# Optimization experiments

Hardware: AMD Instinct MI355X
Metric: run time of the kernel (lower is better)

## Reference

```python
import jax, jax.numpy as jnp
import numpy as np

EPS = 1e-5  # torch BatchNorm2d default eps


def _conv1x1(x, W, b):
    # x: [B,C,H,W], W: [O,C], b: [O]
    return jnp.einsum('bchw,oc->bohw', x, W) + b[None, :, None, None]


def _bn_eval(y, gamma, beta, mean, var):
    inv = gamma / jnp.sqrt(var + EPS)
    return y * inv[None, :, None, None] + (beta - mean * inv)[None, :, None, None]


def setup_inputs() -> dict:
    key = jax.random.key(0)
    ks = jax.random.split(key, 12)
    B, C, H, W = 4, 256, 64, 64
    mid = C // 4  # k = 4
    sc_in = (2.0 / C) ** 0.5   # kaiming_normal fan_in = C for 1x1 conv
    sc_mid = (2.0 / mid) ** 0.5
    x = jax.random.normal(ks[0], (B, C, H, W), jnp.float32)
    Wf = jax.random.normal(ks[1], (mid, C), jnp.float32) * sc_in
    bf = jnp.zeros((mid,), jnp.float32)
    gamma_f = jnp.ones((mid,), jnp.float32)
    beta_f = jnp.zeros((mid,), jnp.float32)
    mean_f = jax.random.normal(ks[2], (mid,), jnp.float32) * 0.1
    var_f = jax.random.uniform(ks[3], (mid,), jnp.float32, 0.5, 1.5)
    Wg = jax.random.normal(ks[4], (mid, C), jnp.float32) * sc_in
    bg = jnp.zeros((mid,), jnp.float32)
    gamma_g = jnp.ones((mid,), jnp.float32)
    beta_g = jnp.zeros((mid,), jnp.float32)
    mean_g = jax.random.normal(ks[5], (mid,), jnp.float32) * 0.1
    var_g = jax.random.uniform(ks[6], (mid,), jnp.float32, 0.5, 1.5)
    Wh = jax.random.normal(ks[7], (mid, C), jnp.float32) * sc_in
    bh = jnp.zeros((mid,), jnp.float32)
    # v conv is constant-initialized to 0 in the original; use small random
    # weights so the attention branch contributes to the output under test.
    Wv = jax.random.normal(ks[8], (C, mid), jnp.float32) * sc_mid * 0.1
    bv = jnp.zeros((C,), jnp.float32)
    v0 = jax.random.normal(ks[9], (B, H * W, 1), jnp.float32)  # power-iter init
    return dict(x=x, Wf=Wf, bf=bf, gamma_f=gamma_f, beta_f=beta_f, mean_f=mean_f,
                var_f=var_f, Wg=Wg, bg=bg, gamma_g=gamma_g, beta_g=beta_g,
                mean_g=mean_g, var_g=var_g, Wh=Wh, bh=bh, Wv=Wv, bv=bv, v0=v0)


def reference(x, Wf, bf, gamma_f, beta_f, mean_f, var_f,
              Wg, bg, gamma_g, beta_g, mean_g, var_g,
              Wh, bh, Wv, bv, v0):
    B, C, H, W = x.shape
    mid = Wf.shape[0]
    HW = H * W
    f_x = jax.nn.relu(_bn_eval(_conv1x1(x, Wf, bf), gamma_f, beta_f, mean_f, var_f)).reshape(B, mid, HW)
    g_x = jax.nn.relu(_bn_eval(_conv1x1(x, Wg, bg), gamma_g, beta_g, mean_g, var_g)).reshape(B, mid, HW)
    h_x = _conv1x1(x, Wh, bh).reshape(B, mid, HW)
    # dense non-local correlation: [B, HW, HW]
    z = jnp.einsum('bcn,bcm->bnm', f_x, g_x)
    # power iteration (Ip=1) for spectral-norm estimate
    v = jnp.einsum('bnm,bmk->bnk', z, v0)          # [B,HW,1]
    v = v / jnp.linalg.norm(v[:, :, 0], axis=1)[:, None, None]
    s = jnp.einsum('bn,bnm,bm->b', v[:, :, 0], z, v[:, :, 0])[:, None, None]
    attn = z / s
    z2 = jnp.einsum('bnm,bcm->bcn', attn, h_x).reshape(B, mid, H, W)
    return _conv1x1(z2, Wv, bv) + x
```

## Files before the change

### kernel.cpp

```cpp
#include <hip/hip_runtime.h>

#define NB   4
#define CIN  256
#define MID  64
#define HW   4096

typedef __attribute__((ext_vector_type(8))) short bfrag8;
typedef __attribute__((ext_vector_type(4))) float facc4;

constexpr size_t OFF_FGHT  = 0;
constexpr size_t OFF_FHI   = 8388608;
constexpr size_t OFF_FLO   = 10485760;
constexpr size_t OFF_WHI   = 12582912;
constexpr size_t OFF_WLO   = 12681216;
constexpr size_t OFF_BEFF  = 12779520;
constexpr size_t OFF_W2HI  = 12780544;
constexpr size_t OFF_W2LO  = 12911616;
constexpr size_t OFF_MPART = 13042688;
constexpr size_t OFF_T     = 17236992;
constexpr size_t OFF_FGVU  = 17238016;
constexpr size_t OFF_NSQ   = 17240064;

__device__ __forceinline__ unsigned short f2bf(float f) {
    union { float f; unsigned u; } v; v.f = f;
    unsigned r = v.u + 0x7FFF + ((v.u >> 16) & 1);
    return (unsigned short)(r >> 16);
}
__device__ __forceinline__ float bf2f(unsigned short h) {
    union { unsigned u; float f; } v; v.u = ((unsigned)h) << 16;
    return v.f;
}
__device__ __forceinline__ void split_bf(float v, unsigned short& hi, unsigned short& lo) {
    hi = f2bf(v);
    lo = f2bf(v - bf2f(hi));
}

__global__ void k_weff(const float* __restrict__ Wf, const float* __restrict__ bf,
                       const float* __restrict__ gf, const float* __restrict__ btf,
                       const float* __restrict__ mf, const float* __restrict__ vf,
                       const float* __restrict__ Wg, const float* __restrict__ bg,
                       const float* __restrict__ gg, const float* __restrict__ btg,
                       const float* __restrict__ mg, const float* __restrict__ vg,
                       const float* __restrict__ Wh, const float* __restrict__ bh,
                       unsigned short* __restrict__ whi, unsigned short* __restrict__ wlo,
                       float* __restrict__ beff) {
    const int o = blockIdx.x;
    const int c = threadIdx.x;
    float w, sh;
    if (o < 64) {
        float inv = gf[o] * rsqrtf(vf[o] + 1e-5f);
        w  = Wf[o * CIN + c] * inv;
        sh = bf[o] * inv + btf[o] - mf[o] * inv;
    } else if (o < 128) {
        int oo = o - 64;
        float inv = gg[oo] * rsqrtf(vg[oo] + 1e-5f);
        w  = Wg[oo * CIN + c] * inv;
        sh = bg[oo] * inv + btg[oo] - mg[oo] * inv;
    } else {
        int oo = o - 128;
        w  = Wh[oo * CIN + c];
        sh = bh[oo];
    }
    unsigned short hi, lo; split_bf(w, hi, lo);
    whi[o * CIN + c] = hi;
    wlo[o * CIN + c] = lo;
    if (c == 0) beff[o] = sh;
}

__launch_bounds__(512)
__global__ void k_fgh2(const float* __restrict__ x,
                       const unsigned short* __restrict__ whi_g,
                       const unsigned short* __restrict__ wlo_g,
                       const float* __restrict__ beff,
                       const float* __restrict__ v0,
                       float* __restrict__ fghT,
                       unsigned short* __restrict__ fhi,
                       unsigned short* __restrict__ flo,
                       float* __restrict__ tvec,
                       float* __restrict__ mpart) {
    __shared__ unsigned short xh[64][72], xl[64][72];
    __shared__ char wbuf[2 * 192 * 72 * 2];
    unsigned short (*wh)[72] = (unsigned short(*)[72])wbuf;
    unsigned short (*wl)[72] = (unsigned short(*)[72])(wbuf + 192 * 72 * 2);

    const int nb = blockIdx.x, b = blockIdx.y;
    const int n0 = nb * 64;
    const int tid = threadIdx.x, l = tid & 63, w = tid >> 6;
    const int wo = w >> 1, wn = w & 1;
    const int lr = l & 15, lk = l >> 4;
    facc4 acc[2][3];
    #pragma unroll
    for (int i = 0; i < 2; ++i)
        #pragma unroll
        for (int j = 0; j < 3; ++j) acc[i][j] = (facc4){0.f, 0.f, 0.f, 0.f};

    const int cr = tid >> 4, nq = tid & 15;

    for (int kc = 0; kc < 4; ++kc) {
        const int c0 = kc * 64;
        {
            const float* xr = x + ((size_t)(b * CIN + c0 + cr * 2)) * HW + n0 + nq * 4;
            float4 va = *(const float4*)xr;
            float4 vb = *(const float4*)(xr + HW);
            #pragma unroll
            for (int i = 0; i < 4; ++i) {
                float fa = (&va.x)[i], fb = (&vb.x)[i];
                unsigned short ha, la, hb, lb;
                split_bf(fa, ha, la);
                split_bf(fb, hb, lb);
                const int n = nq * 4 + i;
                *(unsigned int*)&xh[n][cr * 2] = (unsigned int)ha | ((unsigned int)hb << 16);
                *(unsigned int*)&xl[n][cr * 2] = (unsigned int)la | ((unsigned int)lb << 16);
            }
        }
        {
            #pragma unroll
            for (int k = 0; k < 3; ++k) {
                const int id = tid + k * 512;
                const int orow = id >> 3, cs = id & 7;
                *(bfrag8*)&wh[orow][cs * 8] = *(const bfrag8*)(whi_g + orow * CIN + c0 + cs * 8);
                *(bfrag8*)&wl[orow][cs * 8] = *(const bfrag8*)(wlo_g + orow * CIN + c0 + cs * 8);
            }
        }
        __syncthreads();
        #pragma unroll
        for (int ks = 0; ks < 2; ++ks) {
            bfrag8 ah[2], al[2];
            #pragma unroll
            for (int s = 0; s < 2; ++s) {
                ah[s] = *(const bfrag8*)&xh[wn * 32 + s * 16 + lr][ks * 32 + lk * 8];
                al[s] = *(const bfrag8*)&xl[wn * 32 + s * 16 + lr][ks * 32 + lk * 8];
            }
            #pragma unroll
            for (int so = 0; so < 3; ++so) {
                bfrag8 bh = *(const bfrag8*)&wh[wo * 48 + so * 16 + lr][ks * 32 + lk * 8];
                bfrag8 bl = *(const bfrag8*)&wl[wo * 48 + so * 16 + lr][ks * 32 + lk * 8];
                #pragma unroll
                for (int sn = 0; sn < 2; ++sn) {
                    acc[sn][so] = __builtin_amdgcn_mfma_f32_16x16x32_bf16(ah[sn], bh, acc[sn][so], 0, 0, 0);
                    acc[sn][so] = __builtin_amdgcn_mfma_f32_16x16x32_bf16(ah[sn], bl, acc[sn][so], 0, 0, 0);
                    acc[sn][so] = __builtin_amdgcn_mfma_f32_16x16x32_bf16(al[sn], bh, acc[sn][so], 0, 0, 0);
                }
            }
        }
        __syncthreads();
    }

    float (*mls)[136]  = (float(*)[136])wbuf;
    float (*tred)[64]  = (float(*)[64])(wbuf + 36864);
    float* v0ls        = (float*)xh;

    #pragma unroll
    for (int so = 0; so < 3; ++so) {
        const int o = wo * 48 + so * 16 + lr;
        const float bias = beff[o];
        const bool rl = (o < 128);
        #pragma unroll
        for (int sn = 0; sn < 2; ++sn)
            #pragma unroll
            for (int r = 0; r < 4; ++r) {
                const int nn = wn * 32 + sn * 16 + lk * 4 + r;
                const int n = n0 + nn;
                float v = acc[sn][so][r] + bias;
                if (rl) v = fmaxf(v, 0.0f);
                if (o < 128) fghT[((size_t)(b * HW) + n) * 128 + o] = v;
                if (o < 64) {
                    unsigned short hi, lo; split_bf(v, hi, lo);
                    fhi[((size_t)(b * HW) + n) * MID + o] = hi;
                    flo[((size_t)(b * HW) + n) * MID + o] = lo;
                }
                if (o >= 64) mls[nn][o - 64] = v;
            }
    }
    if (tid < 64) v0ls[tid] = v0[(size_t)b * HW + n0 + tid];
    __syncthreads();

    {
        const int c = tid & 63, ng = tid >> 6;
        float tp = 0.f;
        #pragma unroll
        for (int i = 0; i < 8; ++i) {
            const int nn = ng * 8 + i;
            tp = fmaf(mls[nn][c], v0ls[nn], tp);
        }
        tred[ng][c] = tp;
    }
    {
        const int tcp = tid >> 4, tc = tid & 15;
        const int cp = tcp * 2, cc = tc * 4;
        float macc[2][4];
        #pragma unroll
        for (int i = 0; i < 2; ++i)
            #pragma unroll
            for (int j = 0; j < 4; ++j) macc[i][j] = 0.f;
        for (int nn = 0; nn < 64; ++nn) {
            const float g0 = mls[nn][cp], g1 = mls[nn][cp + 1];
            const float h0 = mls[nn][64 + cc + 0], h1 = mls[nn][64 + cc + 1];
            const float h2 = mls[nn][64 + cc + 2], h3 = mls[nn][64 + cc + 3];
            macc[0][0] = fmaf(g0, h0, macc[0][0]); macc[0][1] = fmaf(g0, h1, macc[0][1]);
            macc[0][2] = fmaf(g0, h2, macc[0][2]); macc[0][3] = fmaf(g0, h3, macc[0][3]);
            macc[1][0] = fmaf(g1, h0, macc[1][0]); macc[1][1] = fmaf(g1, h1, macc[1][1]);
            macc[1][2] = fmaf(g1, h2, macc[1][2]); macc[1][3] = fmaf(g1, h3, macc[1][3]);
        }
        const size_t mpb = ((size_t)(b * 64 + nb) * 64) * 64;
        *(float4*)&mpart[mpb + (size_t)(cp + 0) * 64 + cc] =
            make_float4(macc[0][0], macc[0][1], macc[0][2], macc[0][3]);
        *(float4*)&mpart[mpb + (size_t)(cp + 1) * 64 + cc] =
            make_float4(macc[1][0], macc[1][1], macc[1][2], macc[1][3]);
    }
    __syncthreads();
    if (tid < 64) {
        float s = 0.f;
        #pragma unroll
        for (int g = 0; g < 8; ++g) s += tred[g][tid];
        atomicAdd(&tvec[b * MID + tid], s);
    }
}

__launch_bounds__(256)
__global__ void k_vfg(const float* __restrict__ fghT, const float* __restrict__ t,
                      float* __restrict__ fgvu, float* __restrict__ nsq) {
    __shared__ float ts[64];
    __shared__ float vuls[256];
    __shared__ float red2[8][128];
    __shared__ float rs[4];
    const int b = blockIdx.y, n0 = blockIdx.x * 256;
    const int tid = threadIdx.x;
    if (tid < 64) ts[tid] = t[b * MID + tid];
    __syncthreads();
    const int nl = tid >> 2, q = tid & 3;
    float mynsq = 0.f;
    for (int ps = 0; ps < 4; ++ps) {
        const int n = n0 + ps * 64 + nl;
        const float* p = fghT + ((size_t)(b * HW) + n) * 128 + q * 16;
        float a = 0.f;
        #pragma unroll
        for (int u = 0; u < 4; ++u) {
            float4 fv = *(const float4*)(p + u * 4);
            a = fmaf(fv.x, ts[q * 16 + u * 4 + 0], a);
            a = fmaf(fv.y, ts[q * 16 + u * 4 + 1], a);
            a = fmaf(fv.z, ts[q * 16 + u * 4 + 2], a);
            a = fmaf(fv.w, ts[q * 16 + u * 4 + 3], a);
        }
        a += __shfl_xor(a, 1);
        a += __shfl_xor(a, 2);
        if (q == 0) { vuls[ps * 64 + nl] = a; mynsq += a * a; }
    }
    {
        float s = mynsq;
        #pragma unroll
        for (int off = 32; off > 0; off >>= 1) s += __shfl_down(s, off);
        if ((tid & 63) == 0) rs[tid >> 6] = s;
        __syncthreads();
        if (tid == 0) atomicAdd(&nsq[b], rs[0] + rs[1] + rs[2] + rs[3]);
    }
    const int rq = tid & 31, ng2 = tid >> 5;
    float a2[4] = {0.f, 0.f, 0.f, 0.f};
    for (int it = 0; it < 32; ++it) {
        const int ni = ng2 + 8 * it;
        float4 fv = *(const float4*)(fghT + ((size_t)(b * HW) + n0 + ni) * 128 + rq * 4);
        const float vv = vuls[ni];
        a2[0] = fmaf(fv.x, vv, a2[0]); a2[1] = fmaf(fv.y, vv, a2[1]);
        a2[2] = fmaf(fv.z, vv, a2[2]); a2[3] = fmaf(fv.w, vv, a2[3]);
    }
    #pragma unroll
    for (int i = 0; i < 4; ++i) red2[ng2][rq * 4 + i] = a2[i];
    __syncthreads();
    if (tid < 128) {
        float s = 0.f;
        #pragma unroll
        for (int g = 0; g < 8; ++g) s += red2[g][tid];
        atomicAdd(&fgvu[b * 128 + tid], s);
    }
}

__launch_bounds__(256)
__global__ void k_w2s(const float* __restrict__ Wv, const float* __restrict__ mpart,
                      const float* __restrict__ fgvu, const float* __restrict__ nsq,
                      unsigned short* __restrict__ w2hi, unsigned short* __restrict__ w2lo) {
    __shared__ float Mc[8][64];
    __shared__ float svs;
    const int cp0 = blockIdx.x * 8, b = blockIdx.y;
    const int tid = threadIdx.x;
    {
        const int c = tid & 63;
        const int r0 = tid >> 6, r1 = r0 + 4;
        float s0 = 0.f, s1 = 0.f;
        for (int nb = 0; nb < 64; ++nb) {
            const size_t base = ((size_t)(b * 64 + nb) * 64) * 64;
            s0 += mpart[base + (size_t)(cp0 + r0) * 64 + c];
            s1 += mpart[base + (size_t)(cp0 + r1) * 64 + c];
        }
        Mc[r0][c] = s0;
        Mc[r1][c] = s1;
    }
    if (tid < 64) {
        float a = fgvu[b * 128 + tid] * fgvu[b * 128 + 64 + tid];
        #pragma unroll
        for (int off = 32; off > 0; off >>= 1) a += __shfl_down(a, off);
        if (tid == 0) svs = a / nsq[b];
    }
    __syncthreads();
    const float inv_s = 1.0f / svs;
    const int o = tid;
    float wv[64];
    #pragma unroll
    for (int u = 0; u < 16; ++u) {
        float4 w4 = *(const float4*)(Wv + o * MID + u * 4);
        wv[u * 4 + 0] = w4.x; wv[u * 4 + 1] = w4.y; wv[u * 4 + 2] = w4.z; wv[u * 4 + 3] = w4.w;
    }
    unsigned short rh[8] __attribute__((aligned(16)));
    unsigned short rl[8] __attribute__((aligned(16)));
    #pragma unroll
    for (int j = 0; j < 8; ++j) {
        float a = 0.f;
        #pragma unroll
        for (int c = 0; c < 64; ++c) a = fmaf(wv[c], Mc[j][c], a);
        split_bf(a * inv_s, rh[j], rl[j]);
    }
    const size_t base = ((size_t)(b * CIN) + o) * MID + cp0;
    *(bfrag8*)(w2hi + base) = *(const bfrag8*)rh;
    *(bfrag8*)(w2lo + base) = *(const bfrag8*)rl;
}

__launch_bounds__(256)
__global__ void k_out(const float* __restrict__ x,
                      const unsigned short* __restrict__ fhi, const unsigned short* __restrict__ flo,
                      const unsigned short* __restrict__ w2hi, const unsigned short* __restrict__ w2lo,
                      const float* __restrict__ bv, float* __restrict__ out) {
    __shared__ unsigned short fh[64][72], fl[64][72], wh[64][72], wl[64][72];
    const int n0 = blockIdx.x * 64;
    const int o0 = blockIdx.y * 64;
    const int b  = blockIdx.z;
    const int tid = threadIdx.x, l = tid & 63, w = tid >> 6;
    const int wo = w >> 1, wn = w & 1;
    const int lr = l & 15, lk = l >> 4;
    #pragma unroll
    for (int i = 0; i < 2; ++i) {
        int ch = tid + i * 256;
        int row = ch >> 3, cs = ch & 7;
        const size_t fsrc = ((size_t)(b * HW) + n0 + row) * MID + cs * 8;
        const size_t wsrc = ((size_t)(b * CIN) + o0 + row) * MID + cs * 8;
        *(bfrag8*)&fh[row][cs * 8] = *(const bfrag8*)(fhi + fsrc);
        *(bfrag8*)&fl[row][cs * 8] = *(const bfrag8*)(flo + fsrc);
        *(bfrag8*)&wh[row][cs * 8] = *(const bfrag8*)(w2hi + wsrc);
        *(bfrag8*)&wl[row][cs * 8] = *(const bfrag8*)(w2lo + wsrc);
    }
    __syncthreads();
    facc4 acc[2][2];
    #pragma unroll
    for (int i = 0; i < 2; ++i)
        #pragma unroll
        for (int j = 0; j < 2; ++j) acc[i][j] = (facc4){0.f, 0.f, 0.f, 0.f};
    #pragma unroll
    for (int ks = 0; ks < 2; ++ks) {
        bfrag8 ah[2], al[2], bh[2], bl[2];
        #pragma unroll
        for (int s = 0; s < 2; ++s) {
            ah[s] = *(const bfrag8*)&wh[wo * 32 + s * 16 + lr][ks * 32 + lk * 8];
            al[s] = *(const bfrag8*)&wl[wo * 32 + s * 16 + lr][ks * 32 + lk * 8];
            bh[s] = *(const bfrag8*)&fh[wn * 32 + s * 16 + lr][ks * 32 + lk * 8];
            bl[s] = *(const bfrag8*)&fl[wn * 32 + s * 16 + lr][ks * 32 + lk * 8];
        }
        #pragma unroll
        for (int so = 0; so < 2; ++so)
            #pragma unroll
            for (int sn = 0; sn < 2; ++sn) {
                acc[so][sn] = __builtin_amdgcn_mfma_f32_16x16x32_bf16(ah[so], bh[sn], acc[so][sn], 0, 0, 0);
                acc[so][sn] = __builtin_amdgcn_mfma_f32_16x16x32_bf16(ah[so], bl[sn], acc[so][sn], 0, 0, 0);
                acc[so][sn] = __builtin_amdgcn_mfma_f32_16x16x32_bf16(al[so], bh[sn], acc[so][sn], 0, 0, 0);
            }
    }
    #pragma unroll
    for (int so = 0; so < 2; ++so)
        #pragma unroll
        for (int r = 0; r < 4; ++r) {
            const int o = o0 + wo * 32 + so * 16 + lk * 4 + r;
            const float bias = bv[o];
            #pragma unroll
            for (int sn = 0; sn < 2; ++sn) {
                const int n = n0 + wn * 32 + sn * 16 + lr;
                const size_t idx = ((size_t)(b * CIN) + o) * HW + n;
                out[idx] = x[idx] + bias + acc[so][sn][r];
            }
        }
}

extern "C" void kernel_launch(void* const* d_in, const int* in_sizes, int n_in,
                              void* d_out, int out_size, void* d_ws, size_t ws_size,
                              hipStream_t stream) {
    const float* x   = (const float*)d_in[0];
    const float* Wf  = (const float*)d_in[1];
    const float* bf  = (const float*)d_in[2];
    const float* gaf = (const float*)d_in[3];
    const float* bef = (const float*)d_in[4];
    const float* mef = (const float*)d_in[5];
    const float* vaf = (const float*)d_in[6];
    const float* Wg  = (const float*)d_in[7];
    const float* bg  = (const float*)d_in[8];
    const float* gag = (const float*)d_in[9];
    const float* beg = (const float*)d_in[10];
    const float* meg = (const float*)d_in[11];
    const float* vag = (const float*)d_in[12];
    const float* Wh  = (const float*)d_in[13];
    const float* bh  = (const float*)d_in[14];
    const float* Wv  = (const float*)d_in[15];
    const float* bv  = (const float*)d_in[16];
    const float* v0  = (const float*)d_in[17];
    float* out = (float*)d_out;
    char* ws = (char*)d_ws;

    float*          fghT = (float*)(ws + OFF_FGHT);
    unsigned short* fhi  = (unsigned short*)(ws + OFF_FHI);
    unsigned short* flo  = (unsigned short*)(ws + OFF_FLO);
    unsigned short* whi  = (unsigned short*)(ws + OFF_WHI);
    unsigned short* wlo  = (unsigned short*)(ws + OFF_WLO);
    float*          beff = (float*)(ws + OFF_BEFF);
    unsigned short* w2hi = (unsigned short*)(ws + OFF_W2HI);
    unsigned short* w2lo = (unsigned short*)(ws + OFF_W2LO);
    float*          mpart= (float*)(ws + OFF_MPART);
    float*          tvec = (float*)(ws + OFF_T);
    float*          fgvu = (float*)(ws + OFF_FGVU);
    float*          nsq  = (float*)(ws + OFF_NSQ);

    hipMemsetAsync(tvec, 0, 3328, stream);

    k_weff<<<192, CIN, 0, stream>>>(Wf, bf, gaf, bef, mef, vaf,
                                    Wg, bg, gag, beg, meg, vag,
                                    Wh, bh, whi, wlo, beff);
    k_fgh2<<<dim3(HW / 64, NB), 512, 0, stream>>>(x, whi, wlo, beff, v0,
                                                  fghT, fhi, flo, tvec, mpart);
    k_vfg <<<dim3(16, NB), 256, 0, stream>>>(fghT, tvec, fgvu, nsq);
    k_w2s <<<dim3(8, NB), 256, 0, stream>>>(Wv, mpart, fgvu, nsq, w2hi, w2lo);
    k_out <<<dim3(HW / 64, CIN / 64, NB), 256, 0, stream>>>(x, fhi, flo, w2hi, w2lo, bv, out);
}
```

Before: 138.3 us.

## Replace atomic reductions with partial buffers and widen small reduction kernel grids

The small reduction vectors (t, fgvu, nsq) are now written as per-block partial results instead of being accumulated with atomicAdd, so the hipMemsetAsync that zeroed them is no longer needed. The launch grids of k_vfg and k_w2s are enlarged (64 and 16 blocks per batch) so more of the GPU works on these latency-bound stages. Consumer kernels reduce the partials themselves, which adds some redundant reads in exchange for removing the memset and the atomic contention. This also makes the reductions deterministic.

```diff
diff --git a/kernel.cpp b/kernel.cpp
--- a/kernel.cpp
+++ b/kernel.cpp
@@ -6,6 +6,7 @@
 #define HW   4096
 
 typedef __attribute__((ext_vector_type(8))) short bfrag8;
+typedef __attribute__((ext_vector_type(4))) short svec4;
 typedef __attribute__((ext_vector_type(4))) float facc4;
 
 constexpr size_t OFF_FGHT  = 0;
@@ -17,9 +18,9 @@
 constexpr size_t OFF_W2HI  = 12780544;
 constexpr size_t OFF_W2LO  = 12911616;
 constexpr size_t OFF_MPART = 13042688;
-constexpr size_t OFF_T     = 17236992;
-constexpr size_t OFF_FGVU  = 17238016;
-constexpr size_t OFF_NSQ   = 17240064;
+constexpr size_t OFF_TPART = 17236992;
+constexpr size_t OFF_FGVUP = 17302528;
+constexpr size_t OFF_NSQP  = 17433600;
 
 __device__ __forceinline__ unsigned short f2bf(float f) {
     union { float f; unsigned u; } v; v.f = f;
@@ -76,10 +77,9 @@
                        float* __restrict__ fghT,
                        unsigned short* __restrict__ fhi,
                        unsigned short* __restrict__ flo,
-                       float* __restrict__ tvec,
-                       float* __restrict__ mpart) {
+                       float* __restrict__ tpart, float* __restrict__ mpart) {
     __shared__ unsigned short xh[64][72], xl[64][72];
-    __shared__ char wbuf[2 * 192 * 72 * 2];
+    __shared__ char wbuf[55296];
     unsigned short (*wh)[72] = (unsigned short(*)[72])wbuf;
     unsigned short (*wl)[72] = (unsigned short(*)[72])(wbuf + 192 * 72 * 2);
 
@@ -133,22 +133,22 @@
             }
             #pragma unroll
             for (int so = 0; so < 3; ++so) {
-                bfrag8 bh = *(const bfrag8*)&wh[wo * 48 + so * 16 + lr][ks * 32 + lk * 8];
-                bfrag8 bl = *(const bfrag8*)&wl[wo * 48 + so * 16 + lr][ks * 32 + lk * 8];
+                bfrag8 bh8 = *(const bfrag8*)&wh[wo * 48 + so * 16 + lr][ks * 32 + lk * 8];
+                bfrag8 bl8 = *(const bfrag8*)&wl[wo * 48 + so * 16 + lr][ks * 32 + lk * 8];
                 #pragma unroll
                 for (int sn = 0; sn < 2; ++sn) {
-                    acc[sn][so] = __builtin_amdgcn_mfma_f32_16x16x32_bf16(ah[sn], bh, acc[sn][so], 0, 0, 0);
-                    acc[sn][so] = __builtin_amdgcn_mfma_f32_16x16x32_bf16(ah[sn], bl, acc[sn][so], 0, 0, 0);
-                    acc[sn][so] = __builtin_amdgcn_mfma_f32_16x16x32_bf16(al[sn], bh, acc[sn][so], 0, 0, 0);
+                    acc[sn][so] = __builtin_amdgcn_mfma_f32_16x16x32_bf16(ah[sn], bh8, acc[sn][so], 0, 0, 0);
+                    acc[sn][so] = __builtin_amdgcn_mfma_f32_16x16x32_bf16(ah[sn], bl8, acc[sn][so], 0, 0, 0);
+                    acc[sn][so] = __builtin_amdgcn_mfma_f32_16x16x32_bf16(al[sn], bh8, acc[sn][so], 0, 0, 0);
                 }
             }
         }
         __syncthreads();
     }
 
-    float (*mls)[136]  = (float(*)[136])wbuf;
-    float (*tred)[64]  = (float(*)[64])(wbuf + 36864);
-    float* v0ls        = (float*)xh;
+    float (*mls)[136] = (float(*)[136])wbuf;
+    float (*tred)[64] = (float(*)[64])(wbuf + 36864);
+    float* v0ls       = (float*)xh;
 
     #pragma unroll
     for (int so = 0; so < 3; ++so) {
@@ -213,25 +213,35 @@
         float s = 0.f;
         #pragma unroll
         for (int g = 0; g < 8; ++g) s += tred[g][tid];
-        atomicAdd(&tvec[b * MID + tid], s);
+        tpart[((size_t)(b * 64) + nb) * 64 + tid] = s;
     }
 }
 
 __launch_bounds__(256)
-__global__ void k_vfg(const float* __restrict__ fghT, const float* __restrict__ t,
-                      float* __restrict__ fgvu, float* __restrict__ nsq) {
+__global__ void k_vfg(const float* __restrict__ fghT, const float* __restrict__ tpart,
+                      float* __restrict__ fgvu_part, float* __restrict__ nsq_part) {
+    __shared__ float tred4[4][64];
     __shared__ float ts[64];
-    __shared__ float vuls[256];
+    __shared__ float vuls[64];
     __shared__ float red2[8][128];
     __shared__ float rs[4];
-    const int b = blockIdx.y, n0 = blockIdx.x * 256;
+    const int chunk = blockIdx.x, b = blockIdx.y, n0 = chunk * 64;
     const int tid = threadIdx.x;
-    if (tid < 64) ts[tid] = t[b * MID + tid];
+    {
+        const int c = tid & 63, grp = tid >> 6;
+        float s = 0.f;
+        #pragma unroll
+        for (int i = 0; i < 16; ++i)
+            s += tpart[((size_t)(b * 64) + grp * 16 + i) * 64 + c];
+        tred4[grp][c] = s;
+    }
+    __syncthreads();
+    if (tid < 64) ts[tid] = tred4[0][tid] + tred4[1][tid] + tred4[2][tid] + tred4[3][tid];
     __syncthreads();
     const int nl = tid >> 2, q = tid & 3;
     float mynsq = 0.f;
-    for (int ps = 0; ps < 4; ++ps) {
-        const int n = n0 + ps * 64 + nl;
+    {
+        const int n = n0 + nl;
         const float* p = fghT + ((size_t)(b * HW) + n) * 128 + q * 16;
         float a = 0.f;
         #pragma unroll
@@ -244,7 +254,7 @@
         }
         a += __shfl_xor(a, 1);
         a += __shfl_xor(a, 2);
-        if (q == 0) { vuls[ps * 64 + nl] = a; mynsq += a * a; }
+        if (q == 0) { vuls[nl] = a; mynsq = a * a; }
     }
     {
         float s = mynsq;
@@ -252,11 +262,12 @@
         for (int off = 32; off > 0; off >>= 1) s += __shfl_down(s, off);
         if ((tid & 63) == 0) rs[tid >> 6] = s;
         __syncthreads();
-        if (tid == 0) atomicAdd(&nsq[b], rs[0] + rs[1] + rs[2] + rs[3]);
+        if (tid == 0) nsq_part[b * 64 + chunk] = rs[0] + rs[1] + rs[2] + rs[3];
     }
     const int rq = tid & 31, ng2 = tid >> 5;
     float a2[4] = {0.f, 0.f, 0.f, 0.f};
-    for (int it = 0; it < 32; ++it) {
+    #pragma unroll
+    for (int it = 0; it < 8; ++it) {
         const int ni = ng2 + 8 * it;
         float4 fv = *(const float4*)(fghT + ((size_t)(b * HW) + n0 + ni) * 128 + rq * 4);
         const float vv = vuls[ni];
@@ -270,35 +281,39 @@
         float s = 0.f;
         #pragma unroll
         for (int g = 0; g < 8; ++g) s += red2[g][tid];
-        atomicAdd(&fgvu[b * 128 + tid], s);
+        fgvu_part[(size_t)(b * 64 + chunk) * 128 + tid] = s;
     }
 }
 
 __launch_bounds__(256)
 __global__ void k_w2s(const float* __restrict__ Wv, const float* __restrict__ mpart,
-                      const float* __restrict__ fgvu, const float* __restrict__ nsq,
+                      const float* __restrict__ fgvu_part, const float* __restrict__ nsq_part,
                       unsigned short* __restrict__ w2hi, unsigned short* __restrict__ w2lo) {
-    __shared__ float Mc[8][64];
+    __shared__ float Mc[4][64];
     __shared__ float svs;
-    const int cp0 = blockIdx.x * 8, b = blockIdx.y;
+    const int cp0 = blockIdx.x * 4, b = blockIdx.y;
     const int tid = threadIdx.x;
     {
-        const int c = tid & 63;
-        const int r0 = tid >> 6, r1 = r0 + 4;
-        float s0 = 0.f, s1 = 0.f;
-        for (int nb = 0; nb < 64; ++nb) {
-            const size_t base = ((size_t)(b * 64 + nb) * 64) * 64;
-            s0 += mpart[base + (size_t)(cp0 + r0) * 64 + c];
-            s1 += mpart[base + (size_t)(cp0 + r1) * 64 + c];
-        }
-        Mc[r0][c] = s0;
-        Mc[r1][c] = s1;
+        const int c = tid & 63, r = tid >> 6;
+        float s = 0.f;
+        for (int nb = 0; nb < 64; ++nb)
+            s += mpart[((size_t)(b * 64 + nb) * 64 + cp0 + r) * 64 + c];
+        Mc[r][c] = s;
     }
     if (tid < 64) {
-        float a = fgvu[b * 128 + tid] * fgvu[b * 128 + 64 + tid];
-        #pragma unroll
-        for (int off = 32; off > 0; off >>= 1) a += __shfl_down(a, off);
-        if (tid == 0) svs = a / nsq[b];
+        float fv = 0.f, gv = 0.f;
+        for (int ch = 0; ch < 64; ++ch) {
+            fv += fgvu_part[(size_t)(b * 64 + ch) * 128 + tid];
+            gv += fgvu_part[(size_t)(b * 64 + ch) * 128 + 64 + tid];
+        }
+        float ns = nsq_part[b * 64 + tid];
+        float num = fv * gv;
+        #pragma unroll
+        for (int off = 32; off > 0; off >>= 1) {
+            num += __shfl_down(num, off);
+            ns  += __shfl_down(ns, off);
+        }
+        if (tid == 0) svs = num / ns;
     }
     __syncthreads();
     const float inv_s = 1.0f / svs;
@@ -309,18 +324,18 @@
         float4 w4 = *(const float4*)(Wv + o * MID + u * 4);
         wv[u * 4 + 0] = w4.x; wv[u * 4 + 1] = w4.y; wv[u * 4 + 2] = w4.z; wv[u * 4 + 3] = w4.w;
     }
-    unsigned short rh[8] __attribute__((aligned(16)));
-    unsigned short rl[8] __attribute__((aligned(16)));
-    #pragma unroll
-    for (int j = 0; j < 8; ++j) {
+    unsigned short rh[4] __attribute__((aligned(8)));
+    unsigned short rl[4] __attribute__((aligned(8)));
+    #pragma unroll
+    for (int j = 0; j < 4; ++j) {
         float a = 0.f;
         #pragma unroll
         for (int c = 0; c < 64; ++c) a = fmaf(wv[c], Mc[j][c], a);
         split_bf(a * inv_s, rh[j], rl[j]);
     }
     const size_t base = ((size_t)(b * CIN) + o) * MID + cp0;
-    *(bfrag8*)(w2hi + base) = *(const bfrag8*)rh;
-    *(bfrag8*)(w2lo + base) = *(const bfrag8*)rl;
+    *(svec4*)(w2hi + base) = *(const svec4*)rh;
+    *(svec4*)(w2lo + base) = *(const svec4*)rl;
 }
 
 __launch_bounds__(256)
@@ -419,18 +434,16 @@
     unsigned short* w2hi = (unsigned short*)(ws + OFF_W2HI);
     unsigned short* w2lo = (unsigned short*)(ws + OFF_W2LO);
     float*          mpart= (float*)(ws + OFF_MPART);
-    float*          tvec = (float*)(ws + OFF_T);
-    float*          fgvu = (float*)(ws + OFF_FGVU);
-    float*          nsq  = (float*)(ws + OFF_NSQ);
-
-    hipMemsetAsync(tvec, 0, 3328, stream);
+    float*          tpart= (float*)(ws + OFF_TPART);
+    float*          fgvup= (float*)(ws + OFF_FGVUP);
+    float*          nsqp = (float*)(ws + OFF_NSQP);
 
     k_weff<<<192, CIN, 0, stream>>>(Wf, bf, gaf, bef, mef, vaf,
                                     Wg, bg, gag, beg, meg, vag,
                                     Wh, bh, whi, wlo, beff);
     k_fgh2<<<dim3(HW / 64, NB), 512, 0, stream>>>(x, whi, wlo, beff, v0,
-                                                  fghT, fhi, flo, tvec, mpart);
-    k_vfg <<<dim3(16, NB), 256, 0, stream>>>(fghT, tvec, fgvu, nsq);
-    k_w2s <<<dim3(8, NB), 256, 0, stream>>>(Wv, mpart, fgvu, nsq, w2hi, w2lo);
+                                                  fghT, fhi, flo, tpart, mpart);
+    k_vfg <<<dim3(64, NB), 256, 0, stream>>>(fghT, tpart, fgvup, nsqp);
+    k_w2s <<<dim3(16, NB), 256, 0, stream>>>(Wv, mpart, fgvup, nsqp, w2hi, w2lo);
     k_out <<<dim3(HW / 64, CIN / 64, NB), 256, 0, stream>>>(x, fhi, flo, w2hi, w2lo, bv, out);
 }
```

Measured after the change: 133.2 us. 1.04x faster.
